# Optimization experiments

Hardware: AMD Instinct MI355X
Metric: run time of the kernel (lower is better)

Reference implementation:

```python
import jax, jax.numpy as jnp
import numpy as np

N_NODES = 50000
N_EDGES = 800000
IN_CH = 128
OUT_CH = 32
HEADS = 8
NEG_SLOPE = 0.2


def setup_inputs() -> dict:
    key = jax.random.key(0)
    k1, k2, k3, k4, k5, k6 = jax.random.split(key, 6)
    x = jax.random.normal(k1, (N_NODES, IN_CH), dtype=jnp.float32)
    edge_index = jax.random.randint(k2, (2, N_EDGES), 0, N_NODES, dtype=jnp.int64)
    # Glorot-ish scaled params
    W = jax.random.normal(k3, (IN_CH, HEADS * OUT_CH), dtype=jnp.float32) * (1.0 / np.sqrt(IN_CH))
    att_src = jax.random.normal(k4, (HEADS, OUT_CH), dtype=jnp.float32) * (1.0 / np.sqrt(OUT_CH))
    att_dst = jax.random.normal(k5, (HEADS, OUT_CH), dtype=jnp.float32) * (1.0 / np.sqrt(OUT_CH))
    bias = jax.random.normal(k6, (HEADS * OUT_CH,), dtype=jnp.float32) * 0.01
    return {"x": x, "edge_index": edge_index, "W": W, "att_src": att_src, "att_dst": att_dst, "bias": bias}


def reference(x, edge_index, W, att_src, att_dst, bias):
    N = x.shape[0]
    # PyG GATConv default: add self loops
    loops = jnp.arange(N, dtype=edge_index.dtype)
    src = jnp.concatenate([edge_index[0], loops])  # message source j
    dst = jnp.concatenate([edge_index[1], loops])  # message destination i

    # Linear projection: [N, H, C]
    h = (x @ W).reshape(N, HEADS, OUT_CH)

    # Per-node attention logits per head: [N, H]
    a_src = jnp.einsum('nhc,hc->nh', h, att_src)
    a_dst = jnp.einsum('nhc,hc->nh', h, att_dst)

    # Per-edge scores: [E, H]
    e = jax.nn.leaky_relu(a_src[src] + a_dst[dst], NEG_SLOPE)

    # Segment softmax over edges sharing a destination (self loops guarantee non-empty segments)
    e_max = jax.ops.segment_max(e, dst, num_segments=N)
    e_exp = jnp.exp(e - e_max[dst])
    e_sum = jax.ops.segment_sum(e_exp, dst, num_segments=N)
    alpha = e_exp / (e_sum[dst] + 1e-16)  # [E, H]

    # Weighted message aggregation: [N, H, C] -> concat heads [N, H*C]
    msg = h[src] * alpha[:, :, None]
    out = jax.ops.segment_sum(msg, dst, num_segments=N).reshape(N, HEADS * OUT_CH)
    out = out + bias
    # unlinear = ReLU (act='relu', norm=None)
    return jax.nn.relu(out)
```

## Files before the change

### kernel.cpp

```cpp
#include <hip/hip_runtime.h>

#define IN_CH 128
#define OUT_CH 32
#define HEADS 8
#define HC 256
#define NEG_SLOPE 0.2f

typedef __attribute__((ext_vector_type(8))) short short8;
typedef __attribute__((ext_vector_type(4))) float f32x4;

__device__ __forceinline__ float bflo(unsigned u) { return __uint_as_float(u << 16); }
__device__ __forceinline__ float bfhi(unsigned u) { return __uint_as_float(u & 0xffff0000u); }
__device__ __forceinline__ float bf2f(unsigned short u) { return __uint_as_float(((unsigned)u) << 16); }
__device__ __forceinline__ unsigned short f2bf(float f) {
    unsigned u = __float_as_uint(f);
    u = (u + 0x7fffu + ((u >> 16) & 1u)) >> 16;
    return (unsigned short)u;
}

__global__ __launch_bounds__(256)
void gat_prep(const float* __restrict__ W, unsigned short* __restrict__ Wt)
{
    const int idx = blockIdx.x * 256 + threadIdx.x;
    const int k = idx >> 8;
    const int col = idx & 255;
    Wt[col * IN_CH + k] = f2bf(W[idx]);
}

__global__ __launch_bounds__(256)
void gat_proj_mfma(const float* __restrict__ x, const unsigned short* __restrict__ Wt,
                   const float* __restrict__ attS, const float* __restrict__ attD,
                   unsigned short* __restrict__ h, float* __restrict__ aS,
                   float* __restrict__ aD, int N)
{
    __shared__ unsigned short xs[16 * 136];

    const int tid = threadIdx.x;
    const int lane = tid & 63;
    const int w = tid >> 6;
    const int row0 = blockIdx.x * 16;

    short8 bfr[4][4];
    {
        const unsigned short* wp = Wt + (size_t)(w * 64 + (lane & 15)) * IN_CH
                                      + ((lane >> 4) << 3);
#pragma unroll
        for (int i = 0; i < 4; ++i)
#pragma unroll
            for (int ks = 0; ks < 4; ++ks)
                bfr[ks][i] = *(const short8*)(wp + i * 16 * IN_CH + ks * 32);
    }

    {
        const int srow = tid >> 4;
        const int sseg = tid & 15;
        const int grow = row0 + srow;
        float4 v0 = make_float4(0.f, 0.f, 0.f, 0.f), v1 = v0;
        if (grow < N) {
            const float* xp = x + (size_t)grow * IN_CH + sseg * 8;
            v0 = *(const float4*)xp;
            v1 = *(const float4*)(xp + 4);
        }
        unsigned short* lp = xs + srow * 136 + sseg * 8;
        lp[0] = f2bf(v0.x); lp[1] = f2bf(v0.y); lp[2] = f2bf(v0.z); lp[3] = f2bf(v0.w);
        lp[4] = f2bf(v1.x); lp[5] = f2bf(v1.y); lp[6] = f2bf(v1.z); lp[7] = f2bf(v1.w);
    }
    __syncthreads();

    f32x4 acc[4] = {{0.f,0.f,0.f,0.f},{0.f,0.f,0.f,0.f},{0.f,0.f,0.f,0.f},{0.f,0.f,0.f,0.f}};
#pragma unroll
    for (int ks = 0; ks < 4; ++ks) {
        const short8 a = *(const short8*)&xs[(lane & 15) * 136 + ks * 32 + ((lane >> 4) << 3)];
#pragma unroll
        for (int i = 0; i < 4; ++i)
            acc[i] = __builtin_amdgcn_mfma_f32_16x16x32_bf16(a, bfr[ks][i], acc[i], 0, 0, 0);
    }

    const int rbase = (lane >> 4) << 2;
    float ps[2][4] = {{0.f,0.f,0.f,0.f},{0.f,0.f,0.f,0.f}};
    float pd[2][4] = {{0.f,0.f,0.f,0.f},{0.f,0.f,0.f,0.f}};
#pragma unroll
    for (int i = 0; i < 4; ++i) {
        const int col = w * 64 + i * 16 + (lane & 15);
        const int hp = i >> 1;
        const float asv = attS[(w * 2 + hp) * 32 + (i & 1) * 16 + (lane & 15)];
        const float adv = attD[(w * 2 + hp) * 32 + (i & 1) * 16 + (lane & 15)];
#pragma unroll
        for (int r = 0; r < 4; ++r) {
            const int grow = row0 + rbase + r;
            if (grow < N) h[(size_t)grow * HC + col] = f2bf(acc[i][r]);
            ps[hp][r] = fmaf(acc[i][r], asv, ps[hp][r]);
            pd[hp][r] = fmaf(acc[i][r], adv, pd[hp][r]);
        }
    }
#pragma unroll
    for (int off = 1; off < 16; off <<= 1) {
#pragma unroll
        for (int hp = 0; hp < 2; ++hp)
#pragma unroll
            for (int r = 0; r < 4; ++r) {
                ps[hp][r] += __shfl_xor(ps[hp][r], off, 64);
                pd[hp][r] += __shfl_xor(pd[hp][r], off, 64);
            }
    }
    if ((lane & 15) == 0) {
#pragma unroll
        for (int hp = 0; hp < 2; ++hp)
#pragma unroll
            for (int r = 0; r < 4; ++r) {
                const int grow = row0 + rbase + r;
                if (grow < N) {
                    aS[grow * HEADS + w * 2 + hp] = ps[hp][r];
                    aD[grow * HEADS + w * 2 + hp] = pd[hp][r];
                }
            }
    }
}

__global__ __launch_bounds__(256)
void gat_hist(const int* __restrict__ dst, int* __restrict__ counts, int E)
{
    int i = (blockIdx.x * 256 + threadIdx.x) * 4;
    if (i + 3 < E) {
        const int4 d = *(const int4*)&dst[i];
        atomicAdd(&counts[d.x], 1);
        atomicAdd(&counts[d.y], 1);
        atomicAdd(&counts[d.z], 1);
        atomicAdd(&counts[d.w], 1);
    } else {
        for (; i < E; ++i) atomicAdd(&counts[dst[i]], 1);
    }
}

__global__ __launch_bounds__(256)
void gat_scan1(const int* __restrict__ counts, int* __restrict__ bsum, int n)
{
    __shared__ int ws[4];
    const int t = threadIdx.x;
    const int lane = t & 63;
    const int wid = t >> 6;
    const int idx = blockIdx.x * 1024 + t * 4;
    int4 v = {0, 0, 0, 0};
    if (idx + 3 < n) v = *(const int4*)&counts[idx];
    else {
        if (idx < n)     v.x = counts[idx];
        if (idx + 1 < n) v.y = counts[idx + 1];
        if (idx + 2 < n) v.z = counts[idx + 2];
    }
    int s4 = v.x + v.y + v.z + v.w;
#pragma unroll
    for (int off = 1; off < 64; off <<= 1) s4 += __shfl_xor(s4, off, 64);
    if (lane == 0) ws[wid] = s4;
    __syncthreads();
    if (t == 0) bsum[blockIdx.x] = ws[0] + ws[1] + ws[2] + ws[3];
}

__global__ void gat_scan2(int* __restrict__ bsum, int* __restrict__ offsets, int nb, int n)
{
    const int lane = threadIdx.x;
    const int v = (lane < nb) ? bsum[lane] : 0;
    int inc = v;
#pragma unroll
    for (int off = 1; off < 64; off <<= 1) {
        const int y = __shfl_up(inc, off, 64);
        if (lane >= off) inc += y;
    }
    if (lane < nb) bsum[lane] = inc - v;
    if (lane == 63) offsets[n] = inc;
}

__global__ __launch_bounds__(256)
void gat_scan3(const int* __restrict__ counts, const int* __restrict__ bsum,
               int* __restrict__ offsets, int* __restrict__ cursor, int n)
{
    __shared__ int wsums[4];
    const int t = threadIdx.x;
    const int lane = t & 63;
    const int wid = t >> 6;
    const int idx = blockIdx.x * 1024 + t * 4;
    int4 v = {0, 0, 0, 0};
    if (idx + 3 < n) v = *(const int4*)&counts[idx];
    else {
        if (idx < n)     v.x = counts[idx];
        if (idx + 1 < n) v.y = counts[idx + 1];
        if (idx + 2 < n) v.z = counts[idx + 2];
    }
    const int s4 = v.x + v.y + v.z + v.w;
    int inc = s4;
#pragma unroll
    for (int off = 1; off < 64; off <<= 1) {
        const int y = __shfl_up(inc, off, 64);
        if (lane >= off) inc += y;
    }
    if (lane == 63) wsums[wid] = inc;
    __syncthreads();
    int wbase = 0;
    for (int i = 0; i < wid; ++i) wbase += wsums[i];
    const int base = bsum[blockIdx.x] + wbase + (inc - s4);
    int4 o;
    o.x = base;
    o.y = base + v.x;
    o.z = o.y + v.y;
    o.w = o.z + v.z;
    if (idx + 3 < n) {
        *(int4*)&offsets[idx] = o;
        *(int4*)&cursor[idx] = o;
    } else {
        if (idx < n)     { offsets[idx] = o.x;     cursor[idx] = o.x; }
        if (idx + 1 < n) { offsets[idx + 1] = o.y; cursor[idx + 1] = o.y; }
        if (idx + 2 < n) { offsets[idx + 2] = o.z; cursor[idx + 2] = o.z; }
    }
}

__global__ __launch_bounds__(256)
void gat_scatter(const int* __restrict__ src, const int* __restrict__ dst,
                 int* __restrict__ cursor, int* __restrict__ ssrc,
                 unsigned short* __restrict__ ealpha,
                 const float* __restrict__ aS, const float* __restrict__ aD, int E)
{
    const int e = blockIdx.x * 256 + threadIdx.x;
    if (e >= E) return;
    const int s = src[e];
    const int d = dst[e];
    const int pos = atomicAdd(&cursor[d], 1);
    ssrc[pos] = s;
    const float4 s0 = *(const float4*)(aS + (size_t)s * HEADS);
    const float4 s1 = *(const float4*)(aS + (size_t)s * HEADS + 4);
    const float4 d0 = *(const float4*)(aD + (size_t)d * HEADS);
    const float4 d1 = *(const float4*)(aD + (size_t)d * HEADS + 4);
    float lg[8] = { s0.x + d0.x, s0.y + d0.y, s0.z + d0.z, s0.w + d0.w,
                    s1.x + d1.x, s1.y + d1.y, s1.z + d1.z, s1.w + d1.w };
    short8 al;
#pragma unroll
    for (int k = 0; k < 8; ++k) {
        const float v = lg[k] > 0.f ? lg[k] : NEG_SLOPE * lg[k];
        al[k] = (short)f2bf(__expf(v));
    }
    *(short8*)(ealpha + (size_t)pos * HEADS) = al;
}

__global__ __launch_bounds__(256)
void gat_agg(const unsigned short* __restrict__ h,
             const float* __restrict__ aS, const float* __restrict__ aD,
             const int* __restrict__ offsets, const int* __restrict__ ssrc,
             const unsigned short* __restrict__ ealpha,
             const float* __restrict__ bias, float* __restrict__ out, int N)
{
    const int t = threadIdx.x;
    const int lane = t & 63;
    const int node = blockIdx.x * 4 + (t >> 6);
    if (node >= N) return;

    const int half = lane >> 5;
    const int hl = lane & 31;
    const int head = hl >> 2;
    const int ch = head * 32 + (hl & 3) * 8;

    float sum;
    float acc[8];
    {
        float lg0 = aS[node * HEADS + head] + aD[node * HEADS + head];
        lg0 = (lg0 > 0.f) ? lg0 : NEG_SLOPE * lg0;
        const float w0 = half ? 0.f : __expf(lg0);
        sum = w0;
        const uint4 hv = *(const uint4*)(h + (size_t)node * HC + ch);
        acc[0] = w0 * bflo(hv.x); acc[1] = w0 * bfhi(hv.x);
        acc[2] = w0 * bflo(hv.y); acc[3] = w0 * bfhi(hv.y);
        acc[4] = w0 * bflo(hv.z); acc[5] = w0 * bfhi(hv.z);
        acc[6] = w0 * bflo(hv.w); acc[7] = w0 * bfhi(hv.w);
    }

    const int beg = offsets[node];
    const int end = offsets[node + 1];
    const int last = end - 1;

    int s0 = node, s1 = node;
    float a0 = 0.f, a1 = 0.f;
    if (beg < end) {
        const int e0 = beg + half * 2;
        const int e1 = e0 + 1;
        const int c0 = min(e0, last), c1 = min(e1, last);
        s0 = ssrc[c0]; s1 = ssrc[c1];
        a0 = bf2f(ealpha[(size_t)c0 * HEADS + head]);
        a1 = bf2f(ealpha[(size_t)c1 * HEADS + head]);
        if (e0 > last) { s0 = node; a0 = 0.f; }
        if (e1 > last) { s1 = node; a1 = 0.f; }
    }

#pragma unroll 2
    for (int base = beg; base < end; base += 4) {
        const int n0 = base + 4 + half * 2;
        const int n1 = n0 + 1;
        const int c0 = min(n0, last), c1 = min(n1, last);
        int t0 = ssrc[c0];
        int t1 = ssrc[c1];
        float b0 = bf2f(ealpha[(size_t)c0 * HEADS + head]);
        float b1 = bf2f(ealpha[(size_t)c1 * HEADS + head]);
        if (n0 > last) { t0 = node; b0 = 0.f; }
        if (n1 > last) { t1 = node; b1 = 0.f; }

        const uint4 v0 = *(const uint4*)(h + (size_t)s0 * HC + ch);
        const uint4 v1 = *(const uint4*)(h + (size_t)s1 * HC + ch);
        sum += a0 + a1;
        acc[0] = fmaf(a0, bflo(v0.x), acc[0]);
        acc[1] = fmaf(a0, bfhi(v0.x), acc[1]);
        acc[2] = fmaf(a0, bflo(v0.y), acc[2]);
        acc[3] = fmaf(a0, bfhi(v0.y), acc[3]);
        acc[4] = fmaf(a0, bflo(v0.z), acc[4]);
        acc[5] = fmaf(a0, bfhi(v0.z), acc[5]);
        acc[6] = fmaf(a0, bflo(v0.w), acc[6]);
        acc[7] = fmaf(a0, bfhi(v0.w), acc[7]);
        acc[0] = fmaf(a1, bflo(v1.x), acc[0]);
        acc[1] = fmaf(a1, bfhi(v1.x), acc[1]);
        acc[2] = fmaf(a1, bflo(v1.y), acc[2]);
        acc[3] = fmaf(a1, bfhi(v1.y), acc[3]);
        acc[4] = fmaf(a1, bflo(v1.z), acc[4]);
        acc[5] = fmaf(a1, bfhi(v1.z), acc[5]);
        acc[6] = fmaf(a1, bflo(v1.w), acc[6]);
        acc[7] = fmaf(a1, bfhi(v1.w), acc[7]);
        s0 = t0; s1 = t1; a0 = b0; a1 = b1;
    }

#pragma unroll
    for (int j = 0; j < 8; ++j) acc[j] += __shfl_xor(acc[j], 32, 64);
    sum += __shfl_xor(sum, 32, 64);

    const float inv = 1.f / (sum + 1e-16f);
    const int cbase = ch + half * 4;
    const int j0 = half * 4;
    const float4 bv = *(const float4*)(bias + cbase);
    float4 o;
    o.x = fmaxf(fmaf(acc[j0 + 0], inv, bv.x), 0.f);
    o.y = fmaxf(fmaf(acc[j0 + 1], inv, bv.y), 0.f);
    o.z = fmaxf(fmaf(acc[j0 + 2], inv, bv.z), 0.f);
    o.w = fmaxf(fmaf(acc[j0 + 3], inv, bv.w), 0.f);
    *(float4*)(out + (size_t)node * HC + cbase) = o;
}

extern "C" void kernel_launch(void* const* d_in, const int* in_sizes, int n_in,
                              void* d_out, int out_size, void* d_ws, size_t ws_size,
                              hipStream_t stream)
{
    const float* x    = (const float*)d_in[0];
    const int*   ei   = (const int*)d_in[1];
    const float* W    = (const float*)d_in[2];
    const float* attS = (const float*)d_in[3];
    const float* attD = (const float*)d_in[4];
    const float* bias = (const float*)d_in[5];
    float* out = (float*)d_out;

    const int N = in_sizes[0] / IN_CH;
    const int E = in_sizes[1] / 2;
    const int* esrc = ei;
    const int* edst = ei + E;

    unsigned short* h = (unsigned short*)d_ws;
    float* aS = (float*)(h + (size_t)N * HC);
    float* aD = aS + (size_t)N * HEADS;
    int* counts  = (int*)(aD + (size_t)N * HEADS);
    int* offsets = counts + N;
    int* cursor  = offsets + (N + 4);
    int* ssrc    = cursor + N;
    int* bsum    = ssrc + E;
    unsigned short* Wt = (unsigned short*)(bsum + 64);
    unsigned short* ealpha = Wt + IN_CH * HC;

    const int nb = (N + 1023) / 1024;

    hipMemsetAsync(counts, 0, (size_t)N * sizeof(int), stream);

    gat_prep<<<(IN_CH * HC) / 256, 256, 0, stream>>>(W, Wt);
    gat_proj_mfma<<<(N + 15) / 16, 256, 0, stream>>>(x, Wt, attS, attD, h, aS, aD, N);
    gat_hist<<<(E / 4 + 255) / 256, 256, 0, stream>>>(edst, counts, E);
    gat_scan1<<<nb, 256, 0, stream>>>(counts, bsum, N);
    gat_scan2<<<1, 64, 0, stream>>>(bsum, offsets, nb, N);
    gat_scan3<<<nb, 256, 0, stream>>>(counts, bsum, offsets, cursor, N);
    gat_scatter<<<(E + 255) / 256, 256, 0, stream>>>(esrc, edst, cursor, ssrc, ealpha, aS, aD, E);
    gat_agg<<<(N + 3) / 4, 256, 0, stream>>>(h, aS, aD, offsets, ssrc, ealpha, bias, out, N);
}
```

Baseline: 197.0 us.

## Fold memset and scan2 into other kernels, widen projection tile, deepen agg prefetch

Moves the zeroing of the histogram counts into the weight-prep kernel and folds the single-block block-sum scan into scan3, which removes two launches. The projection kernel now handles 32 rows per block with two MFMA row tiles, so the B fragments loaded from registers are reused twice. The aggregation loop prefetches four edges per half-wave instead of two, which puts more gathers in flight. The cost is more registers in agg and proj, plus redundant per-block scan work in scan3, which assumes nb is at most 64.

```diff
diff --git a/kernel.cpp b/kernel.cpp
--- a/kernel.cpp
+++ b/kernel.cpp
@@ -19,12 +19,14 @@
 }
 
 __global__ __launch_bounds__(256)
-void gat_prep(const float* __restrict__ W, unsigned short* __restrict__ Wt)
+void gat_prep(const float* __restrict__ W, unsigned short* __restrict__ Wt,
+              int* __restrict__ counts, int n)
 {
     const int idx = blockIdx.x * 256 + threadIdx.x;
     const int k = idx >> 8;
     const int col = idx & 255;
     Wt[col * IN_CH + k] = f2bf(W[idx]);
+    for (int i = idx; i < n; i += 32768) counts[i] = 0;
 }
 
 __global__ __launch_bounds__(256)
@@ -33,12 +35,12 @@
                    unsigned short* __restrict__ h, float* __restrict__ aS,
                    float* __restrict__ aD, int N)
 {
-    __shared__ unsigned short xs[16 * 136];
+    __shared__ unsigned short xs[32 * 136];
 
     const int tid = threadIdx.x;
     const int lane = tid & 63;
     const int w = tid >> 6;
-    const int row0 = blockIdx.x * 16;
+    const int row0 = blockIdx.x * 32;
 
     short8 bfr[4][4];
     {
@@ -51,9 +53,11 @@
                 bfr[ks][i] = *(const short8*)(wp + i * 16 * IN_CH + ks * 32);
     }
 
-    {
-        const int srow = tid >> 4;
-        const int sseg = tid & 15;
+#pragma unroll
+    for (int u = 0; u < 2; ++u) {
+        const int unit = tid + u * 256;
+        const int srow = unit >> 4;
+        const int sseg = unit & 15;
         const int grow = row0 + srow;
         float4 v0 = make_float4(0.f, 0.f, 0.f, 0.f), v1 = v0;
         if (grow < N) {
@@ -67,18 +71,33 @@
     }
     __syncthreads();
 
-    f32x4 acc[4] = {{0.f,0.f,0.f,0.f},{0.f,0.f,0.f,0.f},{0.f,0.f,0.f,0.f},{0.f,0.f,0.f,0.f}};
+    f32x4 acc[2][4];
+#pragma unroll
+    for (int m = 0; m < 2; ++m)
+#pragma unroll
+        for (int i = 0; i < 4; ++i) acc[m][i] = (f32x4){0.f, 0.f, 0.f, 0.f};
+
 #pragma unroll
     for (int ks = 0; ks < 4; ++ks) {
-        const short8 a = *(const short8*)&xs[(lane & 15) * 136 + ks * 32 + ((lane >> 4) << 3)];
-#pragma unroll
-        for (int i = 0; i < 4; ++i)
-            acc[i] = __builtin_amdgcn_mfma_f32_16x16x32_bf16(a, bfr[ks][i], acc[i], 0, 0, 0);
+#pragma unroll
+        for (int m = 0; m < 2; ++m) {
+            const short8 a = *(const short8*)&xs[((lane & 15) + m * 16) * 136
+                                                 + ks * 32 + ((lane >> 4) << 3)];
+#pragma unroll
+            for (int i = 0; i < 4; ++i)
+                acc[m][i] = __builtin_amdgcn_mfma_f32_16x16x32_bf16(a, bfr[ks][i], acc[m][i], 0, 0, 0);
+        }
     }
 
     const int rbase = (lane >> 4) << 2;
-    float ps[2][4] = {{0.f,0.f,0.f,0.f},{0.f,0.f,0.f,0.f}};
-    float pd[2][4] = {{0.f,0.f,0.f,0.f},{0.f,0.f,0.f,0.f}};
+    float ps[2][2][4], pd[2][2][4];
+#pragma unroll
+    for (int m = 0; m < 2; ++m)
+#pragma unroll
+        for (int hp = 0; hp < 2; ++hp)
+#pragma unroll
+            for (int r = 0; r < 4; ++r) { ps[m][hp][r] = 0.f; pd[m][hp][r] = 0.f; }
+
 #pragma unroll
     for (int i = 0; i < 4; ++i) {
         const int col = w * 64 + i * 16 + (lane & 15);
@@ -86,34 +105,41 @@
         const float asv = attS[(w * 2 + hp) * 32 + (i & 1) * 16 + (lane & 15)];
         const float adv = attD[(w * 2 + hp) * 32 + (i & 1) * 16 + (lane & 15)];
 #pragma unroll
-        for (int r = 0; r < 4; ++r) {
-            const int grow = row0 + rbase + r;
-            if (grow < N) h[(size_t)grow * HC + col] = f2bf(acc[i][r]);
-            ps[hp][r] = fmaf(acc[i][r], asv, ps[hp][r]);
-            pd[hp][r] = fmaf(acc[i][r], adv, pd[hp][r]);
+        for (int m = 0; m < 2; ++m) {
+#pragma unroll
+            for (int r = 0; r < 4; ++r) {
+                const int grow = row0 + m * 16 + rbase + r;
+                if (grow < N) h[(size_t)grow * HC + col] = f2bf(acc[m][i][r]);
+                ps[m][hp][r] = fmaf(acc[m][i][r], asv, ps[m][hp][r]);
+                pd[m][hp][r] = fmaf(acc[m][i][r], adv, pd[m][hp][r]);
+            }
         }
     }
 #pragma unroll
     for (int off = 1; off < 16; off <<= 1) {
 #pragma unroll
-        for (int hp = 0; hp < 2; ++hp)
-#pragma unroll
-            for (int r = 0; r < 4; ++r) {
-                ps[hp][r] += __shfl_xor(ps[hp][r], off, 64);
-                pd[hp][r] += __shfl_xor(pd[hp][r], off, 64);
-            }
+        for (int m = 0; m < 2; ++m)
+#pragma unroll
+            for (int hp = 0; hp < 2; ++hp)
+#pragma unroll
+                for (int r = 0; r < 4; ++r) {
+                    ps[m][hp][r] += __shfl_xor(ps[m][hp][r], off, 64);
+                    pd[m][hp][r] += __shfl_xor(pd[m][hp][r], off, 64);
+                }
     }
     if ((lane & 15) == 0) {
 #pragma unroll
-        for (int hp = 0; hp < 2; ++hp)
-#pragma unroll
-            for (int r = 0; r < 4; ++r) {
-                const int grow = row0 + rbase + r;
-                if (grow < N) {
-                    aS[grow * HEADS + w * 2 + hp] = ps[hp][r];
-                    aD[grow * HEADS + w * 2 + hp] = pd[hp][r];
+        for (int m = 0; m < 2; ++m)
+#pragma unroll
+            for (int hp = 0; hp < 2; ++hp)
+#pragma unroll
+                for (int r = 0; r < 4; ++r) {
+                    const int grow = row0 + m * 16 + rbase + r;
+                    if (grow < N) {
+                        aS[grow * HEADS + w * 2 + hp] = ps[m][hp][r];
+                        aD[grow * HEADS + w * 2 + hp] = pd[m][hp][r];
+                    }
                 }
-            }
     }
 }
 
@@ -155,28 +181,30 @@
     if (t == 0) bsum[blockIdx.x] = ws[0] + ws[1] + ws[2] + ws[3];
 }
 
-__global__ void gat_scan2(int* __restrict__ bsum, int* __restrict__ offsets, int nb, int n)
-{
-    const int lane = threadIdx.x;
-    const int v = (lane < nb) ? bsum[lane] : 0;
-    int inc = v;
-#pragma unroll
-    for (int off = 1; off < 64; off <<= 1) {
-        const int y = __shfl_up(inc, off, 64);
-        if (lane >= off) inc += y;
-    }
-    if (lane < nb) bsum[lane] = inc - v;
-    if (lane == 63) offsets[n] = inc;
-}
-
 __global__ __launch_bounds__(256)
 void gat_scan3(const int* __restrict__ counts, const int* __restrict__ bsum,
-               int* __restrict__ offsets, int* __restrict__ cursor, int n)
+               int* __restrict__ offsets, int* __restrict__ cursor,
+               int n, int nb, int E)
 {
     __shared__ int wsums[4];
+    __shared__ int bbase_s;
     const int t = threadIdx.x;
     const int lane = t & 63;
     const int wid = t >> 6;
+
+    if (t < 64) {
+        const int v = (t < nb) ? bsum[t] : 0;
+        int inc = v;
+#pragma unroll
+        for (int off = 1; off < 64; off <<= 1) {
+            const int y = __shfl_up(inc, off, 64);
+            if (t >= off) inc += y;
+        }
+        const int myv   = __shfl(v, blockIdx.x, 64);
+        const int myinc = __shfl(inc, blockIdx.x, 64);
+        if (t == 0) bbase_s = myinc - myv;
+    }
+
     const int idx = blockIdx.x * 1024 + t * 4;
     int4 v = {0, 0, 0, 0};
     if (idx + 3 < n) v = *(const int4*)&counts[idx];
@@ -196,7 +224,7 @@
     __syncthreads();
     int wbase = 0;
     for (int i = 0; i < wid; ++i) wbase += wsums[i];
-    const int base = bsum[blockIdx.x] + wbase + (inc - s4);
+    const int base = bbase_s + wbase + (inc - s4);
     int4 o;
     o.x = base;
     o.y = base + v.x;
@@ -210,6 +238,7 @@
         if (idx + 1 < n) { offsets[idx + 1] = o.y; cursor[idx + 1] = o.y; }
         if (idx + 2 < n) { offsets[idx + 2] = o.z; cursor[idx + 2] = o.z; }
     }
+    if (blockIdx.x == 0 && t == 0) offsets[n] = E;
 }
 
 __global__ __launch_bounds__(256)
@@ -274,51 +303,53 @@
     const int end = offsets[node + 1];
     const int last = end - 1;
 
-    int s0 = node, s1 = node;
-    float a0 = 0.f, a1 = 0.f;
+    int sE[4];
+    float aE[4];
+#pragma unroll
+    for (int j = 0; j < 4; ++j) { sE[j] = node; aE[j] = 0.f; }
+
     if (beg < end) {
-        const int e0 = beg + half * 2;
-        const int e1 = e0 + 1;
-        const int c0 = min(e0, last), c1 = min(e1, last);
-        s0 = ssrc[c0]; s1 = ssrc[c1];
-        a0 = bf2f(ealpha[(size_t)c0 * HEADS + head]);
-        a1 = bf2f(ealpha[(size_t)c1 * HEADS + head]);
-        if (e0 > last) { s0 = node; a0 = 0.f; }
-        if (e1 > last) { s1 = node; a1 = 0.f; }
-    }
-
-#pragma unroll 2
-    for (int base = beg; base < end; base += 4) {
-        const int n0 = base + 4 + half * 2;
-        const int n1 = n0 + 1;
-        const int c0 = min(n0, last), c1 = min(n1, last);
-        int t0 = ssrc[c0];
-        int t1 = ssrc[c1];
-        float b0 = bf2f(ealpha[(size_t)c0 * HEADS + head]);
-        float b1 = bf2f(ealpha[(size_t)c1 * HEADS + head]);
-        if (n0 > last) { t0 = node; b0 = 0.f; }
-        if (n1 > last) { t1 = node; b1 = 0.f; }
-
-        const uint4 v0 = *(const uint4*)(h + (size_t)s0 * HC + ch);
-        const uint4 v1 = *(const uint4*)(h + (size_t)s1 * HC + ch);
-        sum += a0 + a1;
-        acc[0] = fmaf(a0, bflo(v0.x), acc[0]);
-        acc[1] = fmaf(a0, bfhi(v0.x), acc[1]);
-        acc[2] = fmaf(a0, bflo(v0.y), acc[2]);
-        acc[3] = fmaf(a0, bfhi(v0.y), acc[3]);
-        acc[4] = fmaf(a0, bflo(v0.z), acc[4]);
-        acc[5] = fmaf(a0, bfhi(v0.z), acc[5]);
-        acc[6] = fmaf(a0, bflo(v0.w), acc[6]);
-        acc[7] = fmaf(a0, bfhi(v0.w), acc[7]);
-        acc[0] = fmaf(a1, bflo(v1.x), acc[0]);
-        acc[1] = fmaf(a1, bfhi(v1.x), acc[1]);
-        acc[2] = fmaf(a1, bflo(v1.y), acc[2]);
-        acc[3] = fmaf(a1, bfhi(v1.y), acc[3]);
-        acc[4] = fmaf(a1, bflo(v1.z), acc[4]);
-        acc[5] = fmaf(a1, bfhi(v1.z), acc[5]);
-        acc[6] = fmaf(a1, bflo(v1.w), acc[6]);
-        acc[7] = fmaf(a1, bfhi(v1.w), acc[7]);
-        s0 = t0; s1 = t1; a0 = b0; a1 = b1;
+#pragma unroll
+        for (int j = 0; j < 4; ++j) {
+            const int e = beg + half * 4 + j;
+            const int c = min(e, last);
+            int s = ssrc[c];
+            float a = bf2f(ealpha[(size_t)c * HEADS + head]);
+            if (e > last) { s = node; a = 0.f; }
+            sE[j] = s; aE[j] = a;
+        }
+    }
+
+    for (int base = beg; base < end; base += 8) {
+        int tS[4]; float tA[4];
+#pragma unroll
+        for (int j = 0; j < 4; ++j) {
+            const int e = base + 8 + half * 4 + j;
+            const int c = min(e, last);
+            int s = ssrc[c];
+            float a = bf2f(ealpha[(size_t)c * HEADS + head]);
+            if (e > last) { s = node; a = 0.f; }
+            tS[j] = s; tA[j] = a;
+        }
+        uint4 v[4];
+#pragma unroll
+        for (int j = 0; j < 4; ++j)
+            v[j] = *(const uint4*)(h + (size_t)sE[j] * HC + ch);
+#pragma unroll
+        for (int j = 0; j < 4; ++j) {
+            const float a = aE[j];
+            sum += a;
+            acc[0] = fmaf(a, bflo(v[j].x), acc[0]);
+            acc[1] = fmaf(a, bfhi(v[j].x), acc[1]);
+            acc[2] = fmaf(a, bflo(v[j].y), acc[2]);
+            acc[3] = fmaf(a, bfhi(v[j].y), acc[3]);
+            acc[4] = fmaf(a, bflo(v[j].z), acc[4]);
+            acc[5] = fmaf(a, bfhi(v[j].z), acc[5]);
+            acc[6] = fmaf(a, bflo(v[j].w), acc[6]);
+            acc[7] = fmaf(a, bfhi(v[j].w), acc[7]);
+        }
+#pragma unroll
+        for (int j = 0; j < 4; ++j) { sE[j] = tS[j]; aE[j] = tA[j]; }
     }
 
 #pragma unroll
@@ -367,14 +398,11 @@
 
     const int nb = (N + 1023) / 1024;
 
-    hipMemsetAsync(counts, 0, (size_t)N * sizeof(int), stream);
-
-    gat_prep<<<(IN_CH * HC) / 256, 256, 0, stream>>>(W, Wt);
-    gat_proj_mfma<<<(N + 15) / 16, 256, 0, stream>>>(x, Wt, attS, attD, h, aS, aD, N);
+    gat_prep<<<(IN_CH * HC) / 256, 256, 0, stream>>>(W, Wt, counts, N);
+    gat_proj_mfma<<<(N + 31) / 32, 256, 0, stream>>>(x, Wt, attS, attD, h, aS, aD, N);
     gat_hist<<<(E / 4 + 255) / 256, 256, 0, stream>>>(edst, counts, E);
     gat_scan1<<<nb, 256, 0, stream>>>(counts, bsum, N);
-    gat_scan2<<<1, 64, 0, stream>>>(bsum, offsets, nb, N);
-    gat_scan3<<<nb, 256, 0, stream>>>(counts, bsum, offsets, cursor, N);
+    gat_scan3<<<nb, 256, 0, stream>>>(counts, bsum, offsets, cursor, N, nb, E);
     gat_scatter<<<(E + 255) / 256, 256, 0, stream>>>(esrc, edst, cursor, ssrc, ealpha, aS, aD, E);
     gat_agg<<<(N + 3) / 4, 256, 0, stream>>>(h, aS, aD, offsets, ssrc, ealpha, bias, out, N);
 }
```

After: 190.0 us. 3.5% less time.
